# Performance work log

Hardware: AMD Instinct MI355X
Metric: run time of the kernel (lower is better)

Reference implementation:

```python
import jax, jax.numpy as jnp
import numpy as np
from jax.scipy.special import erf

N = 4096        # n_points
M = 65536       # number of interaction events
T_MAX = 100.0   # observation window end
BETA0 = 1.0


def setup_inputs() -> dict:
    key = jax.random.key(0)
    k1, k2, k3, k4 = jax.random.split(key, 4)
    # data columns: [node_i, node_j, time] (indices stored as floats, as in the torch code)
    ij = jax.random.randint(k1, (M, 2), 0, N).astype(jnp.float32)
    times = jax.random.uniform(k2, (M,), minval=0.0, maxval=T_MAX)
    data = jnp.concatenate([ij, times[:, None]], axis=1)
    # learned parameters, initialized like the torch module
    z0 = jax.random.uniform(k3, (N, 2), dtype=jnp.float32) * 0.5
    v0 = jax.random.uniform(k4, (N, 2), dtype=jnp.float32) * 0.5
    beta = jnp.full((1, 1), BETA0, dtype=jnp.float32)
    t0 = jnp.float32(0.0)
    tn = jnp.float32(T_MAX)
    return {"data": data, "t0": t0, "tn": tn, "beta": beta, "z0": z0, "v0": v0}


def reference(data, t0, tn, beta, z0, v0):
    b = beta[0, 0]
    times = data[:, 2]                                   # (M,)
    i = jnp.floor(data[:, 0]).astype(jnp.int32)          # (M,)
    j = jnp.floor(data[:, 1]).astype(jnp.int32)          # (M,)

    # --- event term: log lambda_ij(t) = beta - ||z_i(t) - z_j(t)||^2, gathered per event.
    # (Identical to building the dense [N,N,M] tensor and fancy-indexing it.)
    zi = z0[i] + v0[i] * times[:, None]                  # (M,2)
    zj = z0[j] + v0[j] * times[:, None]                  # (M,2)
    d_event = jnp.sum((zi - zj) ** 2, axis=1)            # (M,)
    event_intensity = jnp.sum(b - d_event)

    # --- non-event term: closed-form integral of exp(beta - ||dz + dv*t||^2) over [t0, tn]
    # ||dz + dv t||^2 = a t^2 + bb t + c with a=|dv|^2, bb=2 dz.dv, c=|dz|^2
    dz = z0[:, None, :] - z0[None, :, :]                 # (N,N,2)
    dv = v0[:, None, :] - v0[None, :, :]                 # (N,N,2)
    a = jnp.sum(dv * dv, axis=-1)                        # (N,N)
    bb = 2.0 * jnp.sum(dz * dv, axis=-1)                 # (N,N)
    c = jnp.sum(dz * dz, axis=-1)                        # (N,N)
    a_safe = jnp.maximum(a, 1e-10)
    sqa = jnp.sqrt(a_safe)
    # exponent beta - (c - bb^2/(4a)) <= beta, numerically safe
    pref = (jnp.sqrt(jnp.pi) / (2.0 * sqa)) * jnp.exp(b + bb * bb / (4.0 * a_safe) - c)
    upper = erf(sqa * tn + bb / (2.0 * sqa))
    lower = erf(sqa * t0 + bb / (2.0 * sqa))
    integral = pref * (upper - lower)                    # (N,N)
    triu_mask = jnp.triu(jnp.ones((N, N), dtype=bool), k=1)
    non_event_intensity = jnp.sum(jnp.where(triu_mask, integral, 0.0))

    return event_intensity - non_event_intensity
```

## Files before the change

### kernel.cpp

```cpp
#include <hip/hip_runtime.h>


__device__ __forceinline__ float fast_erf_a(float x) {
    const float ax = __builtin_fabsf(x);
    const float t  = __builtin_amdgcn_rcpf(fmaf(0.3275911f, ax, 1.0f));
    float p = fmaf(t, 1.061405429f, -1.453152027f);
    p = fmaf(t, p, 1.421413741f);
    p = fmaf(t, p, -0.284496736f);
    p = fmaf(t, p, 0.254829592f);
    const float y = fmaf(-t * p, __expf(-ax * ax), 1.0f);
    return __builtin_copysignf(y, x);
}

__device__ __forceinline__ float fast_erf_b(float x) {
    const float ax = __builtin_fabsf(x);
    float p = fmaf(ax, 0.078108f, 0.000972f);
    p = fmaf(ax, p, 0.230389f);
    p = fmaf(ax, p, 0.278393f);
    p = fmaf(ax, p, 1.0f);
    const float w  = __builtin_amdgcn_rcpf(p);
    const float w2 = w * w;
    const float y  = fmaf(-w2, w2, 1.0f);
    return __builtin_copysignf(y, x);
}

__device__ __forceinline__ float erf_small(float x) {
    const float x2 = x * x;
    float p = fmaf(x2, 0.0052239776f, -0.0268661706f);
    p = fmaf(x2, p, 0.1128379167f);
    p = fmaf(x2, p, -0.3761263890f);
    p = fmaf(x2, p, 1.1283791671f);
    return x * p;
}

template<bool T0Z>
__device__ __forceinline__ float pair_eval(float2 zi, float2 vi,
                                           float2 zj, float2 vj,
                                           float t0, float tn, float Kb) {
    const float dzx = zi.x - zj.x, dzy = zi.y - zj.y;
    const float dvx = vi.x - vj.x, dvy = vi.y - vj.y;

    const float a  = fmaf(dvx, dvx, dvy * dvy);
    const float du = fmaf(dzx, dvx, dzy * dvy);
    const float c  = fmaf(dzx, dzx, dzy * dzy);

    const float a_safe = fmaxf(a, 1e-10f);
    const float rsq = __builtin_amdgcn_rsqf(a_safe);
    const float sqa = a_safe * rsq;
    const float u   = du * rsq;

    const float pref  = Kb * rsq * __expf(fmaf(u, u, -c));
    const float upper = fast_erf_b(fmaf(sqa, tn, u));
    const float lower = T0Z ? erf_small(u)
                            : fast_erf_a(fmaf(sqa, t0, u));
    return pref * (upper - lower);
}

__device__ __forceinline__ float block_reduce_add(float v) {
    __shared__ float smem[16];
    #pragma unroll
    for (int off = 32; off > 0; off >>= 1)
        v += __shfl_down(v, off, 64);
    const int lane = threadIdx.x & 63;
    const int wave = threadIdx.x >> 6;
    if (lane == 0) smem[wave] = v;
    __syncthreads();
    if (threadIdx.x == 0) {
        float s = smem[0];
        const int nw = (int)blockDim.x >> 6;
        for (int w = 1; w < nw; ++w) s += smem[w];
        return s;
    }
    return 0.0f;
}

template<bool T0Z>
__device__ __forceinline__ float quad_tile(int r0, int rvalid_lo, int jofs, int N,
                                           const float2* __restrict__ z2,
                                           const float2* __restrict__ v2,
                                           float t0, float tn, float Kb) {
    const int r1 = r0 + 1, r2i = r0 + 2, r3 = r0 + 3;
    const int hi = N - 1;
    const int c0 = min(max(r0, 0), hi), c1 = min(max(r1, 0), hi);
    const int c2 = min(max(r2i, 0), hi), c3 = min(max(r3, 0), hi);

    const float2 zr0 = z2[c0], vr0 = v2[c0];
    const float2 zr1 = z2[c1], vr1 = v2[c1];
    const float2 zr2 = z2[c2], vr2 = v2[c2];
    const float2 zr3 = z2[c3], vr3 = v2[c3];

    const int BIG = 0x7fffffff;
    const int m0 = (r0  >= rvalid_lo && r0  < N) ? r0  : BIG;
    const int m1 = (r1  >= rvalid_lo && r1  < N) ? r1  : BIG;
    const int m2 = (r2i >= rvalid_lo && r2i < N) ? r2i : BIG;
    const int m3 = (r3  >= rvalid_lo && r3  < N) ? r3  : BIG;

    float s0 = 0.0f, s1 = 0.0f, s2 = 0.0f, s3 = 0.0f;
    for (int j = r0 + 1 + jofs; j < N; j += 1024) {
        const float2 zj = z2[j], vj = v2[j];
        const float e0 = pair_eval<T0Z>(zr0, vr0, zj, vj, t0, tn, Kb);
        const float e1 = pair_eval<T0Z>(zr1, vr1, zj, vj, t0, tn, Kb);
        const float e2 = pair_eval<T0Z>(zr2, vr2, zj, vj, t0, tn, Kb);
        const float e3 = pair_eval<T0Z>(zr3, vr3, zj, vj, t0, tn, Kb);
        s0 += (j > m0) ? e0 : 0.0f;
        s1 += (j > m1) ? e1 : 0.0f;
        s2 += (j > m2) ? e2 : 0.0f;
        s3 += (j > m3) ? e3 : 0.0f;
    }
    return (s0 + s1) + (s2 + s3);
}

__global__ void __launch_bounds__(256)
fused_kernel(const float* __restrict__ data,
             const float* __restrict__ t0p,
             const float* __restrict__ tnp,
             const float* __restrict__ beta,
             const float* __restrict__ z0,
             const float* __restrict__ v0,
             float* __restrict__ ws, int M, int N) {
    const float t0 = t0p[0];
    const float tn = tnp[0];
    const float b  = beta[0];
    const float Kb = 0.88622692545275801f * __expf(b);
    const float2* __restrict__ z2 = (const float2*)z0;
    const float2* __restrict__ v2 = (const float2*)v0;

    const int ntiles  = (N + 7) / 8;
    const int q       = (int)blockIdx.x >> 2;
    const int jofs    = (((int)blockIdx.x & 3) << 8) + (int)threadIdx.x;
    const int rlow    = 4 * q;
    const int rhigh   = N - 4 - rlow;
    const int hilimit = 4 * ntiles;
    float acc;
    if (t0 == 0.0f) {
        float s = quad_tile<true >(rlow,  0,       jofs, N, z2, v2, t0, tn, Kb);
        s      += quad_tile<true >(rhigh, hilimit, jofs, N, z2, v2, t0, tn, Kb);
        acc = -s;
    } else {
        float s = quad_tile<false>(rlow,  0,       jofs, N, z2, v2, t0, tn, Kb);
        s      += quad_tile<false>(rhigh, hilimit, jofs, N, z2, v2, t0, tn, Kb);
        acc = -s;
    }

    const int chunk = (M + (int)gridDim.x - 1) / (int)gridDim.x;
    const int mbeg  = (int)blockIdx.x * chunk;
    const int mend  = min(mbeg + chunk, M);
    for (int m = mbeg + (int)threadIdx.x; m < mend; m += 256) {
        const float fi = data[3 * m + 0];
        const float fj = data[3 * m + 1];
        const float t  = data[3 * m + 2];
        const int ii = (int)fi;
        const int jj = (int)fj;
        const float2 zi = z2[ii], zj = z2[jj];
        const float2 vi = v2[ii], vj = v2[jj];
        const float dx = (zi.x - zj.x) + (vi.x - vj.x) * t;
        const float dy = (zi.y - zj.y) + (vi.y - vj.y) * t;
        acc += b - (dx * dx + dy * dy);
    }

    const float s = block_reduce_add(acc);
    if (threadIdx.x == 0) ws[blockIdx.x] = s;
}

__global__ void __launch_bounds__(1024)
finalize_kernel(const float* __restrict__ ws, float* __restrict__ out,
                int nblocks) {
    const float4* __restrict__ ws4 = (const float4*)ws;
    const int n4 = nblocks >> 2;
    float v = 0.0f;
    for (int k = threadIdx.x; k < n4; k += 1024) {
        const float4 p = ws4[k];
        v += (p.x + p.y) + (p.z + p.w);
    }
    if (threadIdx.x == 0)
        for (int k = n4 << 2; k < nblocks; ++k) v += ws[k];
    const float s = block_reduce_add(v);
    if (threadIdx.x == 0) out[0] = s;
}

extern "C" void kernel_launch(void* const* d_in, const int* in_sizes, int n_in,
                              void* d_out, int out_size, void* d_ws, size_t ws_size,
                              hipStream_t stream) {
    const float* data = (const float*)d_in[0];
    const float* t0   = (const float*)d_in[1];
    const float* tn   = (const float*)d_in[2];
    const float* beta = (const float*)d_in[3];
    const float* z0   = (const float*)d_in[4];
    const float* v0   = (const float*)d_in[5];
    float* out = (float*)d_out;
    float* ws  = (float*)d_ws;

    const int M = in_sizes[0] / 3;
    const int N = in_sizes[4] / 2;

    const int ntiles = (N + 7) / 8;
    const int blocks = 4 * ntiles;
    fused_kernel<<<blocks, 256, 0, stream>>>(data, t0, tn, beta, z0, v0, ws, M, N);
    finalize_kernel<<<1, 1024, 0, stream>>>(ws, out, blocks);
}
```

Measured before the change: 77.17 us.

## Use 8-row register tiles with peeled triangular boundary and fewer blocks

New measurement: 77.97 us. Within noise of the previous version (+1.0%).

```diff
diff --git a/kernel.cpp b/kernel.cpp
--- a/kernel.cpp
+++ b/kernel.cpp
@@ -34,9 +34,10 @@
 }
 
 template<bool T0Z>
-__device__ __forceinline__ float pair_eval(float2 zi, float2 vi,
-                                           float2 zj, float2 vj,
-                                           float t0, float tn, float Kb) {
+__device__ __forceinline__ void pair_core(float2 zi, float2 vi,
+                                          float2 zj, float2 vj,
+                                          float t0, float tn, float Kb,
+                                          float& pref, float& diff) {
     const float dzx = zi.x - zj.x, dzy = zi.y - zj.y;
     const float dvx = vi.x - vj.x, dvy = vi.y - vj.y;
 
@@ -49,11 +50,29 @@
     const float sqa = a_safe * rsq;
     const float u   = du * rsq;
 
-    const float pref  = Kb * rsq * __expf(fmaf(u, u, -c));
+    pref = Kb * rsq * __expf(fmaf(u, u, -c));
     const float upper = fast_erf_b(fmaf(sqa, tn, u));
     const float lower = T0Z ? erf_small(u)
                             : fast_erf_a(fmaf(sqa, t0, u));
-    return pref * (upper - lower);
+    diff = upper - lower;
+}
+
+template<bool T0Z>
+__device__ __forceinline__ float pair_acc(float acc, float2 zi, float2 vi,
+                                          float2 zj, float2 vj,
+                                          float t0, float tn, float Kb) {
+    float pref, diff;
+    pair_core<T0Z>(zi, vi, zj, vj, t0, tn, Kb, pref, diff);
+    return fmaf(pref, diff, acc);
+}
+
+template<bool T0Z>
+__device__ __forceinline__ float pair_term(float2 zi, float2 vi,
+                                           float2 zj, float2 vj,
+                                           float t0, float tn, float Kb) {
+    float pref, diff;
+    pair_core<T0Z>(zi, vi, zj, vj, t0, tn, Kb, pref, diff);
+    return pref * diff;
 }
 
 __device__ __forceinline__ float block_reduce_add(float v) {
@@ -74,6 +93,53 @@
     return 0.0f;
 }
 
+
+template<bool T0Z>
+__device__ __forceinline__ float octet_boundary(int r0, int j,
+        const float2* __restrict__ z2, const float2* __restrict__ v2,
+        float t0, float tn, float Kb) {
+    const float2 zj = z2[j], vj = v2[j];
+    float s = 0.0f;
+    #pragma unroll
+    for (int k = 0; k < 7; ++k) {
+        const int r = r0 + k;
+        const float e = pair_term<T0Z>(z2[r], v2[r], zj, vj, t0, tn, Kb);
+        s += (j > r) ? e : 0.0f;
+    }
+    return s;
+}
+
+template<bool T0Z>
+__device__ __forceinline__ float octet_main(int r0, int jofs, int N,
+        const float2* __restrict__ z2, const float2* __restrict__ v2,
+        float t0, float tn, float Kb) {
+    const float2 zr0 = z2[r0+0], vr0 = v2[r0+0];
+    const float2 zr1 = z2[r0+1], vr1 = v2[r0+1];
+    const float2 zr2 = z2[r0+2], vr2 = v2[r0+2];
+    const float2 zr3 = z2[r0+3], vr3 = v2[r0+3];
+    const float2 zr4 = z2[r0+4], vr4 = v2[r0+4];
+    const float2 zr5 = z2[r0+5], vr5 = v2[r0+5];
+    const float2 zr6 = z2[r0+6], vr6 = v2[r0+6];
+    const float2 zr7 = z2[r0+7], vr7 = v2[r0+7];
+
+    float s0 = 0.0f, s1 = 0.0f, s2 = 0.0f, s3 = 0.0f;
+    float s4 = 0.0f, s5 = 0.0f, s6 = 0.0f, s7 = 0.0f;
+    #pragma unroll 1
+    for (int j = r0 + 8 + jofs; j < N; j += 1024) {
+        const float2 zj = z2[j], vj = v2[j];
+        s0 = pair_acc<T0Z>(s0, zr0, vr0, zj, vj, t0, tn, Kb);
+        s1 = pair_acc<T0Z>(s1, zr1, vr1, zj, vj, t0, tn, Kb);
+        s2 = pair_acc<T0Z>(s2, zr2, vr2, zj, vj, t0, tn, Kb);
+        s3 = pair_acc<T0Z>(s3, zr3, vr3, zj, vj, t0, tn, Kb);
+        s4 = pair_acc<T0Z>(s4, zr4, vr4, zj, vj, t0, tn, Kb);
+        s5 = pair_acc<T0Z>(s5, zr5, vr5, zj, vj, t0, tn, Kb);
+        s6 = pair_acc<T0Z>(s6, zr6, vr6, zj, vj, t0, tn, Kb);
+        s7 = pair_acc<T0Z>(s7, zr7, vr7, zj, vj, t0, tn, Kb);
+    }
+    return ((s0 + s1) + (s2 + s3)) + ((s4 + s5) + (s6 + s7));
+}
+
+
 template<bool T0Z>
 __device__ __forceinline__ float quad_tile(int r0, int rvalid_lo, int jofs, int N,
                                            const float2* __restrict__ z2,
@@ -83,12 +149,10 @@
     const int hi = N - 1;
     const int c0 = min(max(r0, 0), hi), c1 = min(max(r1, 0), hi);
     const int c2 = min(max(r2i, 0), hi), c3 = min(max(r3, 0), hi);
-
     const float2 zr0 = z2[c0], vr0 = v2[c0];
     const float2 zr1 = z2[c1], vr1 = v2[c1];
     const float2 zr2 = z2[c2], vr2 = v2[c2];
     const float2 zr3 = z2[c3], vr3 = v2[c3];
-
     const int BIG = 0x7fffffff;
     const int m0 = (r0  >= rvalid_lo && r0  < N) ? r0  : BIG;
     const int m1 = (r1  >= rvalid_lo && r1  < N) ? r1  : BIG;
@@ -96,12 +160,13 @@
     const int m3 = (r3  >= rvalid_lo && r3  < N) ? r3  : BIG;
 
     float s0 = 0.0f, s1 = 0.0f, s2 = 0.0f, s3 = 0.0f;
-    for (int j = r0 + 1 + jofs; j < N; j += 1024) {
+    const int jb = max(r0 + 1, 0);
+    for (int j = jb + jofs; j < N; j += 1024) {
         const float2 zj = z2[j], vj = v2[j];
-        const float e0 = pair_eval<T0Z>(zr0, vr0, zj, vj, t0, tn, Kb);
-        const float e1 = pair_eval<T0Z>(zr1, vr1, zj, vj, t0, tn, Kb);
-        const float e2 = pair_eval<T0Z>(zr2, vr2, zj, vj, t0, tn, Kb);
-        const float e3 = pair_eval<T0Z>(zr3, vr3, zj, vj, t0, tn, Kb);
+        const float e0 = pair_term<T0Z>(zr0, vr0, zj, vj, t0, tn, Kb);
+        const float e1 = pair_term<T0Z>(zr1, vr1, zj, vj, t0, tn, Kb);
+        const float e2 = pair_term<T0Z>(zr2, vr2, zj, vj, t0, tn, Kb);
+        const float e3 = pair_term<T0Z>(zr3, vr3, zj, vj, t0, tn, Kb);
         s0 += (j > m0) ? e0 : 0.0f;
         s1 += (j > m1) ? e1 : 0.0f;
         s2 += (j > m2) ? e2 : 0.0f;
@@ -125,27 +190,71 @@
     const float2* __restrict__ z2 = (const float2*)z0;
     const float2* __restrict__ v2 = (const float2*)v0;
 
-    const int ntiles  = (N + 7) / 8;
-    const int q       = (int)blockIdx.x >> 2;
-    const int jofs    = (((int)blockIdx.x & 3) << 8) + (int)threadIdx.x;
-    const int rlow    = 4 * q;
-    const int rhigh   = N - 4 - rlow;
-    const int hilimit = 4 * ntiles;
-    float acc;
-    if (t0 == 0.0f) {
-        float s = quad_tile<true >(rlow,  0,       jofs, N, z2, v2, t0, tn, Kb);
-        s      += quad_tile<true >(rhigh, hilimit, jofs, N, z2, v2, t0, tn, Kb);
-        acc = -s;
-    } else {
-        float s = quad_tile<false>(rlow,  0,       jofs, N, z2, v2, t0, tn, Kb);
-        s      += quad_tile<false>(rhigh, hilimit, jofs, N, z2, v2, t0, tn, Kb);
-        acc = -s;
-    }
+    const int q    = (int)blockIdx.x >> 2;
+    const int jofs = (((int)blockIdx.x & 3) << 8) + (int)threadIdx.x;
+    const int r0   = 8 * q;
+    const int rh   = N - 8 - r0;
 
     const int chunk = (M + (int)gridDim.x - 1) / (int)gridDim.x;
     const int mbeg  = (int)blockIdx.x * chunk;
     const int mend  = min(mbeg + chunk, M);
-    for (int m = mbeg + (int)threadIdx.x; m < mend; m += 256) {
+    const int m0    = mbeg + (int)threadIdx.x;
+    const bool hasev = m0 < mend;
+    float fi0 = 0.0f, fj0 = 0.0f, ft0 = 0.0f;
+    if (hasev) {
+        fi0 = data[3 * m0 + 0];
+        fj0 = data[3 * m0 + 1];
+        ft0 = data[3 * m0 + 2];
+    }
+
+    float s;
+    if ((N & 15) == 0) {
+        if (t0 == 0.0f) {
+            float acc = 0.0f;
+            if (jofs < 7) {
+                acc += octet_boundary<true >(r0, r0 + 1 + jofs, z2, v2, t0, tn, Kb);
+                acc += octet_boundary<true >(rh, rh + 1 + jofs, z2, v2, t0, tn, Kb);
+            }
+            acc += octet_main<true >(r0, jofs, N, z2, v2, t0, tn, Kb);
+            acc += octet_main<true >(rh, jofs, N, z2, v2, t0, tn, Kb);
+            s = acc;
+        } else {
+            float acc = 0.0f;
+            if (jofs < 7) {
+                acc += octet_boundary<false>(r0, r0 + 1 + jofs, z2, v2, t0, tn, Kb);
+                acc += octet_boundary<false>(rh, rh + 1 + jofs, z2, v2, t0, tn, Kb);
+            }
+            acc += octet_main<false>(r0, jofs, N, z2, v2, t0, tn, Kb);
+            acc += octet_main<false>(rh, jofs, N, z2, v2, t0, tn, Kb);
+            s = acc;
+        }
+    } else {
+        const int ntiles  = (N + 15) >> 4;
+        const int hilimit = 8 * ntiles;
+        if (t0 == 0.0f) {
+            s  = quad_tile<true >(r0,     0,       jofs, N, z2, v2, t0, tn, Kb);
+            s += quad_tile<true >(r0 + 4, 0,       jofs, N, z2, v2, t0, tn, Kb);
+            s += quad_tile<true >(rh,     hilimit, jofs, N, z2, v2, t0, tn, Kb);
+            s += quad_tile<true >(rh + 4, hilimit, jofs, N, z2, v2, t0, tn, Kb);
+        } else {
+            s  = quad_tile<false>(r0,     0,       jofs, N, z2, v2, t0, tn, Kb);
+            s += quad_tile<false>(r0 + 4, 0,       jofs, N, z2, v2, t0, tn, Kb);
+            s += quad_tile<false>(rh,     hilimit, jofs, N, z2, v2, t0, tn, Kb);
+            s += quad_tile<false>(rh + 4, hilimit, jofs, N, z2, v2, t0, tn, Kb);
+        }
+    }
+    float acc = -s;
+
+    if (hasev) {
+        const int ii = (int)fi0;
+        const int jj = (int)fj0;
+        const float2 zi = z2[ii], zj = z2[jj];
+        const float2 vi = v2[ii], vj = v2[jj];
+        const float dx = (zi.x - zj.x) + (vi.x - vj.x) * ft0;
+        const float dy = (zi.y - zj.y) + (vi.y - vj.y) * ft0;
+        acc += b - (dx * dx + dy * dy);
+    }
+    for (int m = m0 + 256; m < mend; m += 256) {
         const float fi = data[3 * m + 0];
         const float fj = data[3 * m + 1];
         const float t  = data[3 * m + 2];
@@ -158,8 +267,8 @@
         acc += b - (dx * dx + dy * dy);
     }
 
-    const float s = block_reduce_add(acc);
-    if (threadIdx.x == 0) ws[blockIdx.x] = s;
+    const float sred = block_reduce_add(acc);
+    if (threadIdx.x == 0) ws[blockIdx.x] = sred;
 }
 
 __global__ void __launch_bounds__(1024)
@@ -193,7 +302,7 @@
     const int M = in_sizes[0] / 3;
     const int N = in_sizes[4] / 2;
 
-    const int ntiles = (N + 7) / 8;
+    const int ntiles = (N + 15) / 16;
     const int blocks = 4 * ntiles;
     fused_kernel<<<blocks, 256, 0, stream>>>(data, t0, tn, beta, z0, v0, ws, M, N);
     finalize_kernel<<<1, 1024, 0, stream>>>(ws, out, blocks);
```
